# Kernel optimization log

Hardware: AMD Instinct MI355X
Metric: run time of the kernel (lower is better)

## Reference

```python
import jax, jax.numpy as jnp
import numpy as np

N = 20000      # total nodes
E = 320000     # edges (before self loops)
B = 8          # graphs in batch
F_IN = 100
HID = 256
HEADS = 4
DIMS = [(256, 256), (256, 128), (128, 64), (64, 32)]  # (in_dim, out_dim) per level
NEG_SLOPE = 0.2
LN_EPS = 1e-5


def _glorot(k, shape):
    fan = shape[0] + shape[-1]
    return jax.random.normal(k, shape, jnp.float32) * jnp.sqrt(2.0 / fan)


def setup_inputs() -> dict:
    key = jax.random.key(0)
    ks = jax.random.split(key, 32)
    inp = {}
    inp["x"] = jax.random.normal(ks[0], (N, F_IN), jnp.float32)
    inp["edge_index"] = jax.random.randint(ks[1], (2, E), 0, N)
    inp["batch"] = jnp.sort(jax.random.randint(ks[2], (N,), 0, B))
    inp["W_in"] = _glorot(ks[3], (F_IN, HID))
    inp["b_in"] = jnp.zeros((HID,), jnp.float32)
    i = 4
    for l, (di, do) in enumerate(DIMS):
        inp[f"W{l}"] = _glorot(ks[i], (di, HEADS * do)); i += 1
        inp[f"as{l}"] = _glorot(ks[i], (HEADS, do)); i += 1
        inp[f"ad{l}"] = _glorot(ks[i], (HEADS, do)); i += 1
        inp[f"b{l}"] = jnp.zeros((do,), jnp.float32)
        inp[f"g{l}"] = jnp.ones((do,), jnp.float32)
        inp[f"be{l}"] = jnp.zeros((do,), jnp.float32)
    inp["W_out"] = _glorot(ks[i], (DIMS[-1][1], 1))
    inp["b_out"] = jnp.zeros((1,), jnp.float32)
    return inp


def _gat(x, src, dst, W, a_s, a_d, b):
    # PyG GATConv, heads=HEADS, concat=False (head mean), bias after mean
    h = (x @ W).reshape(N, HEADS, -1)              # [N,H,C]
    al_s = (h * a_s).sum(-1)                        # [N,H]
    al_d = (h * a_d).sum(-1)                        # [N,H]
    e = jax.nn.leaky_relu(al_s[src] + al_d[dst], NEG_SLOPE)  # [Etot,H]
    m = jax.ops.segment_max(e, dst, num_segments=N)
    m = jnp.where(jnp.isfinite(m), m, 0.0)
    ex = jnp.exp(e - m[dst])
    den = jax.ops.segment_sum(ex, dst, num_segments=N)
    alpha = ex / (den[dst] + 1e-16)                 # segment softmax over incoming edges
    out = jax.ops.segment_sum(alpha[:, :, None] * h[src], dst, num_segments=N)
    return out.mean(axis=1) + b                     # [N,C]


def _ln(x, g, b):
    mu = x.mean(-1, keepdims=True)
    var = ((x - mu) ** 2).mean(-1, keepdims=True)
    return (x - mu) * jax.lax.rsqrt(var + LN_EPS) * g + b


def _forward(x, edge_index, batch, W_in, b_in, level_params, W_out, b_out):
    loop = jnp.arange(N)
    src = jnp.concatenate([edge_index[0], loop])    # add self loops (GATConv default)
    dst = jnp.concatenate([edge_index[1], loop])
    h = jax.nn.relu(x @ W_in + b_in)
    for (di, do), (W, a_s, a_d, b, g, be) in zip(DIMS, level_params):
        out = _gat(h, src, dst, W, a_s, a_d, b)
        out = jax.nn.relu(out)
        out = _ln(out, g, be)
        # dropout is identity in eval mode
        if di == do:
            out = out + h
        h = out
    cnt = jax.ops.segment_sum(jnp.ones((N,), h.dtype), batch, num_segments=B)
    pooled = jax.ops.segment_sum(h, batch, num_segments=B) / jnp.maximum(cnt, 1.0)[:, None]
    return (pooled @ W_out + b_out)[:, 0]           # [B]


def reference(x, edge_index, batch, W_in, b_in,
              W0, as0, ad0, b0, g0, be0,
              W1, as1, ad1, b1, g1, be1,
              W2, as2, ad2, b2, g2, be2,
              W3, as3, ad3, b3, g3, be3,
              W_out, b_out):
    level_params = [
        (W0, as0, ad0, b0, g0, be0),
        (W1, as1, ad1, b1, g1, be1),
        (W2, as2, ad2, b2, g2, be2),
        (W3, as3, ad3, b3, g3, be3),
    ]
    return _forward(x, edge_index, batch, W_in, b_in, level_params, W_out, b_out)
```

## Files before the change

kernel.cpp:

```cpp
#include <hip/hip_runtime.h>
#include <hip/hip_bf16.h>
#include <cstdint>

constexpr int NN   = 20000;
constexpr int NNP  = 20032;
constexpr int NE   = 320000;
constexpr int ETOT = NE + NN;
constexpr int BG   = 8;
constexpr int FIN  = 100;
constexpr int HID  = 256;
constexpr int H    = 4;
constexpr float SLOPE  = 0.2f;
constexpr float LN_EPS = 1e-5f;

#define DEVFN __device__ __forceinline__

typedef __bf16 bf16x8 __attribute__((ext_vector_type(8)));
typedef float  f32x4  __attribute__((ext_vector_type(4)));
typedef float  f32x2  __attribute__((ext_vector_type(2)));

DEVFN float lrelu(float v) { return v > 0.f ? v : SLOPE * v; }
DEVFN ushort f2bf(float f) {
    unsigned u = __float_as_uint(f);
    return (ushort)((u + 0x7fffu + ((u >> 16) & 1u)) >> 16);
}
DEVFN float bf_lo(unsigned u) { return __uint_as_float(u << 16); }
DEVFN float bf_hi(unsigned u) { return __uint_as_float(u & 0xffff0000u); }
DEVFN float bf2f(unsigned u) { return __uint_as_float(u << 16); }

__global__ void zero_u32(uint32_t* __restrict__ p, int n) {
    int i = blockIdx.x * blockDim.x + threadIdx.x;
    if (i < n) p[i] = 0u;
}

__global__ void scan_kernel(const int* __restrict__ deg, int* __restrict__ rowptr) {
    __shared__ int wsum[16];
    __shared__ int woff[16];
    __shared__ int ctot;
    const int lane = threadIdx.x & 63;
    const int wv   = threadIdx.x >> 6;
    int carry = 0;
    for (int base = 0; base < NN; base += 1024) {
        int i = base + threadIdx.x;
        int v = (i < NN) ? deg[i] : 0;
        int s = v;
#pragma unroll
        for (int off = 1; off < 64; off <<= 1) {
            int t = __shfl_up(s, off);
            if (lane >= off) s += t;
        }
        if (lane == 63) wsum[wv] = s;
        __syncthreads();
        if (wv == 0 && lane < 16) {
            int ws = wsum[lane];
            int sc = ws;
#pragma unroll
            for (int off = 1; off < 16; off <<= 1) {
                int t = __shfl_up(sc, off);
                if (lane >= off) sc += t;
            }
            woff[lane] = sc - ws;
            if (lane == 15) ctot = sc;
        }
        __syncthreads();
        if (i < NN) rowptr[i] = carry + woff[wv] + (s - v);
        carry += ctot;
        __syncthreads();
    }
    if (threadIdx.x == 0) rowptr[NN] = carry;
}

__global__ void scatter_edges(const int* __restrict__ ei, const int* __restrict__ rowptr,
                              int* __restrict__ fill, int* __restrict__ esrc) {
    int k = blockIdx.x * blockDim.x + threadIdx.x;
    if (k >= ETOT) return;
    int s, d;
    if (k < NE) { s = ei[k]; d = ei[NE + k]; }
    else        { s = k - NE; d = k - NE; }
    int pos = rowptr[d] + atomicAdd(&fill[d], 1);
    esrc[pos] = s;
}

constexpr int CXN  = NN * 128;
constexpr int CWI  = 256 * 128;
constexpr int CW0  = 1024 * 256;
constexpr int CW1  = 512 * 256;
constexpr int CW2  = 256 * 128;
constexpr int CW3  = 128 * 64;
constexpr int CTOT = CXN + CWI + CW0 + CW1 + CW2 + CW3;
constexpr int CALL = CTOT + ETOT;

__global__ void conv_all(const float* __restrict__ x, const float* __restrict__ Wi,
                         const float* __restrict__ W0, const float* __restrict__ W1,
                         const float* __restrict__ W2, const float* __restrict__ W3,
                         const int* __restrict__ ei, int* __restrict__ deg,
                         ushort* __restrict__ xpad, ushort* __restrict__ wti,
                         ushort* __restrict__ wt0, ushort* __restrict__ wt1,
                         ushort* __restrict__ wt2, ushort* __restrict__ wt3) {
    int id = blockIdx.x * blockDim.x + threadIdx.x;
    if (id < CXN) {
        int n = id >> 7, k = id & 127;
        xpad[id] = (k < FIN) ? f2bf(x[(size_t)n * FIN + k]) : (ushort)0;
        return;
    }
    id -= CXN;
    if (id < CWI) { int n = id / 128, k = id - n * 128;
        wti[id] = (k < FIN) ? f2bf(Wi[(size_t)k * 256 + n]) : (ushort)0; return; }
    id -= CWI;
    if (id < CW0) { int n = id / 256, k = id - n * 256;
        wt0[id] = f2bf(W0[(size_t)k * 1024 + n]); return; }
    id -= CW0;
    if (id < CW1) { int n = id / 256, k = id - n * 256;
        wt1[id] = f2bf(W1[(size_t)k * 512 + n]); return; }
    id -= CW1;
    if (id < CW2) { int n = id / 128, k = id - n * 128;
        wt2[id] = f2bf(W2[(size_t)k * 256 + n]); return; }
    id -= CW2;
    if (id < CW3) { int n = id / 64, k = id - n * 64;
        wt3[id] = f2bf(W3[(size_t)k * 128 + n]); return; }
    id -= CW3;
    if (id < ETOT) {
        int d = (id < NE) ? ei[NE + id] : (id - NE);
        atomicAdd(&deg[d], 1);
    }
}

template <int K, int NC, int CT, bool BR, bool AL>
__launch_bounds__(256)
__global__ void gemm_mfma(const ushort* __restrict__ A, const ushort* __restrict__ Wt,
                          const float* __restrict__ bias, void* __restrict__ Cout,
                          const float* __restrict__ a_s, const float* __restrict__ a_d,
                          float* __restrict__ al_s, float* __restrict__ al_d, int M) {
    constexpr int LDK = K + 8;
    constexpr int DO_AL = NC / H;
    __shared__ ushort Bs[64 * LDK];
    const int row0 = blockIdx.x * 64;
    const int colbase = blockIdx.y * (64 * CT);
    const int tid = threadIdx.x;
    constexpr int CH = K / 8;
    const int wave = tid >> 6;
    const int lane = tid & 63;
    const int m = lane & 15;
    const int q = lane >> 4;
    const ushort* Ap  = A + (size_t)(row0 + wave * 16 + m) * K + q * 8;
    const ushort* bp0 = &Bs[(0 * 16 + m) * LDK + q * 8];
    const ushort* bp1 = &Bs[(1 * 16 + m) * LDK + q * 8];
    const ushort* bp2 = &Bs[(2 * 16 + m) * LDK + q * 8];
    const ushort* bp3 = &Bs[(3 * 16 + m) * LDK + q * 8];
    const int grow0 = row0 + wave * 16 + q * 4;

    for (int ct = 0; ct < CT; ct++) {
        const int col0 = colbase + ct * 64;
        for (int c = tid; c < 64 * CH; c += 256) {
            int r = c / CH, cc = c - r * CH;
            *(uint4*)(&Bs[r * LDK + cc * 8]) =
                *(const uint4*)(Wt + (size_t)(col0 + r) * K + cc * 8);
        }
        __syncthreads();
        f32x4 acc0 = {0.f, 0.f, 0.f, 0.f}, acc1 = acc0, acc2 = acc0, acc3 = acc0;
#pragma unroll
        for (int kk = 0; kk < K / 32; kk++) {
            bf16x8 a = *(const bf16x8*)(Ap + kk * 32);
            acc0 = __builtin_amdgcn_mfma_f32_16x16x32_bf16(a, *(const bf16x8*)(bp0 + kk * 32), acc0, 0, 0, 0);
            acc1 = __builtin_amdgcn_mfma_f32_16x16x32_bf16(a, *(const bf16x8*)(bp1 + kk * 32), acc1, 0, 0, 0);
            acc2 = __builtin_amdgcn_mfma_f32_16x16x32_bf16(a, *(const bf16x8*)(bp2 + kk * 32), acc2, 0, 0, 0);
            acc3 = __builtin_amdgcn_mfma_f32_16x16x32_bf16(a, *(const bf16x8*)(bp3 + kk * 32), acc3, 0, 0, 0);
        }
        if (!AL) {
            ushort* Cb = (ushort*)Cout + (size_t)grow0 * NC + col0 + m;
            float b0 = 0, b1 = 0, b2 = 0, b3 = 0;
            if (BR) {
                b0 = bias[col0 + m];      b1 = bias[col0 + m + 16];
                b2 = bias[col0 + m + 32]; b3 = bias[col0 + m + 48];
            }
#pragma unroll
            for (int r = 0; r < 4; r++) {
                if (grow0 + r < M) {
                    float v0 = acc0[r], v1 = acc1[r], v2 = acc2[r], v3 = acc3[r];
                    if (BR) {
                        v0 = fmaxf(v0 + b0, 0.f); v1 = fmaxf(v1 + b1, 0.f);
                        v2 = fmaxf(v2 + b2, 0.f); v3 = fmaxf(v3 + b3, 0.f);
                    }
                    Cb[(size_t)r * NC + 0]  = f2bf(v0);
                    Cb[(size_t)r * NC + 16] = f2bf(v1);
                    Cb[(size_t)r * NC + 32] = f2bf(v2);
                    Cb[(size_t)r * NC + 48] = f2bf(v3);
                }
            }
        } else {
            uchar* Cb = (uchar*)Cout + (size_t)grow0 * NC + col0 + m;
#pragma unroll
            for (int r = 0; r < 4; r++) {
                if (grow0 + r < M) {
                    int pk01 = __builtin_amdgcn_cvt_pk_fp8_f32(acc0[r], acc1[r], 0, false);
                    int pk23 = __builtin_amdgcn_cvt_pk_fp8_f32(acc2[r], acc3[r], 0, false);
                    Cb[(size_t)r * NC + 0]  = (uchar)(pk01 & 0xff);
                    Cb[(size_t)r * NC + 16] = (uchar)((pk01 >> 8) & 0xff);
                    Cb[(size_t)r * NC + 32] = (uchar)(pk23 & 0xff);
                    Cb[(size_t)r * NC + 48] = (uchar)((pk23 >> 8) & 0xff);
                }
            }
            float asv[4], adv[4];
#pragma unroll
            for (int t = 0; t < 4; t++) {
                int gc = col0 + m + 16 * t;
                asv[t] = a_s[gc];
                adv[t] = a_d[gc];
            }
            const int h_lo = col0 / DO_AL;
            const int h_hi = (col0 + 32) / DO_AL;
#pragma unroll
            for (int r = 0; r < 4; r++) {
                float ps0 = acc0[r] * asv[0] + acc1[r] * asv[1];
                float ps1 = acc2[r] * asv[2] + acc3[r] * asv[3];
                float pd0 = acc0[r] * adv[0] + acc1[r] * adv[1];
                float pd1 = acc2[r] * adv[2] + acc3[r] * adv[3];
#pragma unroll
                for (int off = 1; off < 16; off <<= 1) {
                    ps0 += __shfl_xor(ps0, off);
                    ps1 += __shfl_xor(ps1, off);
                    pd0 += __shfl_xor(pd0, off);
                    pd1 += __shfl_xor(pd1, off);
                }
                if (m == 0 && grow0 + r < M) {
                    if (h_lo == h_hi) {
                        atomicAdd(&al_s[(grow0 + r) * H + h_lo], ps0 + ps1);
                        atomicAdd(&al_d[(grow0 + r) * H + h_lo], pd0 + pd1);
                    } else {
                        atomicAdd(&al_s[(grow0 + r) * H + h_lo], ps0);
                        atomicAdd(&al_s[(grow0 + r) * H + h_hi], ps1);
                        atomicAdd(&al_d[(grow0 + r) * H + h_lo], pd0);
                        atomicAdd(&al_d[(grow0 + r) * H + h_hi], pd1);
                    }
                }
            }
        }
        __syncthreads();
    }
}

__global__ void softmax_csr(const int* __restrict__ rowptr, const int* __restrict__ esrc,
                            const float* __restrict__ al_s, const float* __restrict__ al_d,
                            float4* __restrict__ alpha) {
    int wid = (blockIdx.x * blockDim.x + threadIdx.x) >> 6;
    int lane = threadIdx.x & 63;
    if (wid >= NN) return;
    int p0 = rowptr[wid], p1 = rowptr[wid + 1];
    float4 d4 = ((const float4*)al_d)[wid];
    float m0 = -1e30f, m1 = -1e30f, m2 = -1e30f, m3 = -1e30f;
    for (int p = p0 + lane; p < p1; p += 64) {
        int s = esrc[p];
        float4 s4 = ((const float4*)al_s)[s];
        m0 = fmaxf(m0, lrelu(s4.x + d4.x));
        m1 = fmaxf(m1, lrelu(s4.y + d4.y));
        m2 = fmaxf(m2, lrelu(s4.z + d4.z));
        m3 = fmaxf(m3, lrelu(s4.w + d4.w));
    }
#pragma unroll
    for (int off = 32; off > 0; off >>= 1) {
        m0 = fmaxf(m0, __shfl_xor(m0, off));
        m1 = fmaxf(m1, __shfl_xor(m1, off));
        m2 = fmaxf(m2, __shfl_xor(m2, off));
        m3 = fmaxf(m3, __shfl_xor(m3, off));
    }
    float s0 = 0.f, s1 = 0.f, s2 = 0.f, s3 = 0.f;
    for (int p = p0 + lane; p < p1; p += 64) {
        int s = esrc[p];
        float4 s4 = ((const float4*)al_s)[s];
        s0 += __expf(lrelu(s4.x + d4.x) - m0);
        s1 += __expf(lrelu(s4.y + d4.y) - m1);
        s2 += __expf(lrelu(s4.z + d4.z) - m2);
        s3 += __expf(lrelu(s4.w + d4.w) - m3);
    }
#pragma unroll
    for (int off = 32; off > 0; off >>= 1) {
        s0 += __shfl_xor(s0, off);
        s1 += __shfl_xor(s1, off);
        s2 += __shfl_xor(s2, off);
        s3 += __shfl_xor(s3, off);
    }
    float i0 = 0.25f / (s0 + 1e-16f), i1 = 0.25f / (s1 + 1e-16f);
    float i2 = 0.25f / (s2 + 1e-16f), i3 = 0.25f / (s3 + 1e-16f);
    for (int p = p0 + lane; p < p1; p += 64) {
        int s = esrc[p];
        float4 s4 = ((const float4*)al_s)[s];
        alpha[p] = make_float4(__expf(lrelu(s4.x + d4.x) - m0) * i0,
                               __expf(lrelu(s4.y + d4.y) - m1) * i1,
                               __expf(lrelu(s4.z + d4.z) - m2) * i2,
                               __expf(lrelu(s4.w + d4.w) - m3) * i3);
    }
}

template <int DO, bool RESID>
__launch_bounds__(256)
__global__ void aggregate(const uchar* __restrict__ hproj, const int* __restrict__ rowptr,
                          const int* __restrict__ esrc, const float4* __restrict__ alpha,
                          const float* __restrict__ bias, const float* __restrict__ gamma,
                          const float* __restrict__ beta, const ushort* __restrict__ hprev,
                          ushort* __restrict__ hout) {
    constexpr int HDO = H * DO;
    constexpr int SL  = HDO / 16;
    constexpr int EPI = 64 / SL;
    constexpr int HL  = DO / 16;
    const int wave = threadIdx.x >> 6;
    const int lane = threadIdx.x & 63;
    const int n = blockIdx.x * 4 + wave;
    const int e  = lane / SL;
    const int sl = lane - e * SL;
    const int hsel = sl / HL;
    const int p0 = rowptr[n], p1 = rowptr[n + 1];
    const uint4* hp4 = (const uint4*)hproj;

    f32x2 acc2[8];
#pragma unroll
    for (int j = 0; j < 8; j++) acc2[j] = f32x2{0.f, 0.f};

    auto sel = [&](float4 al) {
        return (hsel == 0) ? al.x : (hsel == 1) ? al.y : (hsel == 2) ? al.z : al.w;
    };
    auto consume = [&](uint4 v, float a) {
        f32x2 ap = {a, a};
        acc2[0] += ap * __builtin_amdgcn_cvt_pk_f32_fp8(v.x, false);
        acc2[1] += ap * __builtin_amdgcn_cvt_pk_f32_fp8(v.x, true);
        acc2[2] += ap * __builtin_amdgcn_cvt_pk_f32_fp8(v.y, false);
        acc2[3] += ap * __builtin_amdgcn_cvt_pk_f32_fp8(v.y, true);
        acc2[4] += ap * __builtin_amdgcn_cvt_pk_f32_fp8(v.z, false);
        acc2[5] += ap * __builtin_amdgcn_cvt_pk_f32_fp8(v.z, true);
        acc2[6] += ap * __builtin_amdgcn_cvt_pk_f32_fp8(v.w, false);
        acc2[7] += ap * __builtin_amdgcn_cvt_pk_f32_fp8(v.w, true);
    };

    int p = p0 + e;
    bool va = p < p1;
    bool vb = (p + EPI) < p1;
    float aa = 0.f, ab = 0.f;
    uint4 ua = make_uint4(0, 0, 0, 0), ub = make_uint4(0, 0, 0, 0);
    if (va) { aa = sel(alpha[p]);       ua = hp4[(size_t)esrc[p] * SL + sl]; }
    if (vb) { ab = sel(alpha[p + EPI]); ub = hp4[(size_t)esrc[p + EPI] * SL + sl]; }

    while (__any(va)) {
        int pa = p + 2 * EPI, pb = p + 3 * EPI;
        bool va2 = pa < p1, vb2 = pb < p1;
        float aa2 = 0.f, ab2 = 0.f;
        uint4 ua2 = make_uint4(0, 0, 0, 0), ub2 = make_uint4(0, 0, 0, 0);
        if (va2) { aa2 = sel(alpha[pa]); ua2 = hp4[(size_t)esrc[pa] * SL + sl]; }
        if (vb2) { ab2 = sel(alpha[pb]); ub2 = hp4[(size_t)esrc[pb] * SL + sl]; }
        if (va) consume(ua, aa);
        if (vb) consume(ub, ab);
        p = pa; va = va2; vb = vb2; aa = aa2; ab = ab2; ua = ua2; ub = ub2;
    }

    float acc[16];
#pragma unroll
    for (int j = 0; j < 8; j++) { acc[2 * j] = acc2[j][0]; acc[2 * j + 1] = acc2[j][1]; }

#pragma unroll
    for (int off = 32; off >= HL; off >>= 1) {
#pragma unroll
        for (int j = 0; j < 16; j++) acc[j] += __shfl_xor(acc[j], off);
    }
    const int c2 = lane & (HL - 1);
    const int cb = c2 * 16;
    float val[16];
    float s = 0.f;
    {
        float4 b0 = *(const float4*)(bias + cb);
        float4 b1 = *(const float4*)(bias + cb + 4);
        float4 b2 = *(const float4*)(bias + cb + 8);
        float4 b3 = *(const float4*)(bias + cb + 12);
        float bb[16] = {b0.x, b0.y, b0.z, b0.w, b1.x, b1.y, b1.z, b1.w,
                        b2.x, b2.y, b2.z, b2.w, b3.x, b3.y, b3.z, b3.w};
#pragma unroll
        for (int j = 0; j < 16; j++) {
            val[j] = fmaxf(acc[j] + bb[j], 0.f);
            s += val[j];
        }
    }
#pragma unroll
    for (int off = 1; off < HL; off <<= 1) s += __shfl_xor(s, off);
    float mu = s / DO;
    float q = 0.f;
#pragma unroll
    for (int j = 0; j < 16; j++) {
        val[j] -= mu;
        q += val[j] * val[j];
    }
#pragma unroll
    for (int off = 1; off < HL; off <<= 1) q += __shfl_xor(q, off);
    float rstd = rsqrtf(q / DO + LN_EPS);

    if (lane < HL) {
        float4 g0 = *(const float4*)(gamma + cb);
        float4 g1 = *(const float4*)(gamma + cb + 4);
        float4 g2 = *(const float4*)(gamma + cb + 8);
        float4 g3 = *(const float4*)(gamma + cb + 12);
        float4 e0 = *(const float4*)(beta + cb);
        float4 e1 = *(const float4*)(beta + cb + 4);
        float4 e2 = *(const float4*)(beta + cb + 8);
        float4 e3 = *(const float4*)(beta + cb + 12);
        float gg[16] = {g0.x, g0.y, g0.z, g0.w, g1.x, g1.y, g1.z, g1.w,
                        g2.x, g2.y, g2.z, g2.w, g3.x, g3.y, g3.z, g3.w};
        float ee[16] = {e0.x, e0.y, e0.z, e0.w, e1.x, e1.y, e1.z, e1.w,
                        e2.x, e2.y, e2.z, e2.w, e3.x, e3.y, e3.z, e3.w};
        float o[16];
#pragma unroll
        for (int j = 0; j < 16; j++) o[j] = val[j] * rstd * gg[j] + ee[j];
        if (RESID) {
            const uint4* pv = (const uint4*)(hprev + (size_t)n * DO + cb);
            uint4 r0 = pv[0], r1 = pv[1];
            unsigned rr[8] = {r0.x, r0.y, r0.z, r0.w, r1.x, r1.y, r1.z, r1.w};
#pragma unroll
            for (int j = 0; j < 8; j++) {
                o[2 * j]     += bf_lo(rr[j]);
                o[2 * j + 1] += bf_hi(rr[j]);
            }
        }
        unsigned w[8];
#pragma unroll
        for (int j = 0; j < 8; j++)
            w[j] = (unsigned)f2bf(o[2 * j]) | ((unsigned)f2bf(o[2 * j + 1]) << 16);
        uint4* op = (uint4*)(hout + (size_t)n * DO + cb);
        op[0] = make_uint4(w[0], w[1], w[2], w[3]);
        op[1] = make_uint4(w[4], w[5], w[6], w[7]);
    }
}

__global__ void pool_accum2(const ushort* __restrict__ h, const int* __restrict__ batch,
                            float* __restrict__ pooled, float* __restrict__ cnt) {
    __shared__ float lp[BG * 32];
    __shared__ float lc[BG];
    for (int i = threadIdx.x; i < BG * 32; i += blockDim.x) lp[i] = 0.f;
    if (threadIdx.x < BG) lc[threadIdx.x] = 0.f;
    __syncthreads();
    int c = threadIdx.x & 31;
    int rb = threadIdx.x >> 5;
    for (int n = blockIdx.x * 8 + rb; n < NN; n += gridDim.x * 8) {
        int b = batch[n];
        atomicAdd(&lp[b * 32 + c], bf2f((unsigned)h[(size_t)n * 32 + c]));
        if (c == 0) atomicAdd(&lc[b], 1.f);
    }
    __syncthreads();
    for (int i = threadIdx.x; i < BG * 32; i += blockDim.x) atomicAdd(&pooled[i], lp[i]);
    if (threadIdx.x < BG) atomicAdd(&cnt[threadIdx.x], lc[threadIdx.x]);
}

__global__ void final_out(const float* __restrict__ pooled, const float* __restrict__ cnt,
                          const float* __restrict__ Wo, const float* __restrict__ bo,
                          float* __restrict__ out) {
    int b = threadIdx.x;
    if (b < BG) {
        float inv = 1.f / fmaxf(cnt[b], 1.f);
        float acc = 0.f;
        for (int c = 0; c < 32; c++) acc += pooled[b * 32 + c] * inv * Wo[c];
        out[b] = acc + bo[0];
    }
}

extern "C" void kernel_launch(void* const* d_in, const int* in_sizes, int n_in,
                              void* d_out, int out_size, void* d_ws, size_t ws_size,
                              hipStream_t stream) {
    const float* x     = (const float*)d_in[0];
    const int*   ei    = (const int*)d_in[1];
    const int*   batch = (const int*)d_in[2];
    const float* Wi    = (const float*)d_in[3];
    const float* bi    = (const float*)d_in[4];
    const float* Wl[4]  = {(const float*)d_in[5],  (const float*)d_in[11], (const float*)d_in[17], (const float*)d_in[23]};
    const float* Asl[4] = {(const float*)d_in[6],  (const float*)d_in[12], (const float*)d_in[18], (const float*)d_in[24]};
    const float* Adl[4] = {(const float*)d_in[7],  (const float*)d_in[13], (const float*)d_in[19], (const float*)d_in[25]};
    const float* Bl[4]  = {(const float*)d_in[8],  (const float*)d_in[14], (const float*)d_in[20], (const float*)d_in[26]};
    const float* Gl[4]  = {(const float*)d_in[9],  (const float*)d_in[15], (const float*)d_in[21], (const float*)d_in[27]};
    const float* Bel[4] = {(const float*)d_in[10], (const float*)d_in[16], (const float*)d_in[22], (const float*)d_in[28]};
    const float* Wo = (const float*)d_in[29];
    const float* bo = (const float*)d_in[30];

    char* p = (char*)d_ws;
    auto take = [&](size_t bytes) -> void* {
        void* r = (void*)p;
        p += (bytes + 255) & ~(size_t)255;
        return r;
    };
    ushort*   hAbf   = (ushort*)take((size_t)NNP * HID * 2);
    ushort*   hBbf   = (ushort*)take((size_t)NNP * HID * 2);
    uchar*    hproj  = (uchar*)take((size_t)NN * H * HID);
    ushort*   xpad   = (ushort*)take((size_t)NNP * 128 * 2);
    int*      rowptr = (int*)take((size_t)(NN + 1) * 4);
    int*      esrc   = (int*)take((size_t)ETOT * 4);
    float4*   alpha  = (float4*)take((size_t)ETOT * 16);
    ushort*   wti    = (ushort*)take((size_t)CWI * 2);
    ushort*   wt0    = (ushort*)take((size_t)CW0 * 2);
    ushort*   wt1    = (ushort*)take((size_t)CW1 * 2);
    ushort*   wt2    = (ushort*)take((size_t)CW2 * 2);
    ushort*   wt3    = (ushort*)take((size_t)CW3 * 2);
    char*     zbase  = p;
    int*      deg    = (int*)take((size_t)NN * 4);
    int*      fill   = (int*)take((size_t)NN * 4);
    float*    pooled = (float*)take((size_t)BG * 32 * 4);
    float*    cnt    = (float*)take((size_t)BG * 4);
    float*    als[4], *ald[4];
    for (int l = 0; l < 4; l++) {
        als[l] = (float*)take((size_t)NN * H * 4);
        ald[l] = (float*)take((size_t)NN * H * 4);
    }
    const int zcount = (int)((p - zbase) / 4);
    (void)ws_size; (void)n_in; (void)in_sizes; (void)out_size;

    const int ZB = 256;
    const int egrid = (ETOT + ZB - 1) / ZB;
    const int mtiles = (NN + 63) / 64;
    const int sgrid = (NN * 64 + 255) / 256;
    const int agrid = NN / 4;

    zero_u32<<<(zcount + ZB - 1) / ZB, ZB, 0, stream>>>((uint32_t*)zbase, zcount);
    conv_all<<<(CALL + ZB - 1) / ZB, ZB, 0, stream>>>(x, Wi, Wl[0], Wl[1], Wl[2], Wl[3],
                                                      ei, deg,
                                                      xpad, wti, wt0, wt1, wt2, wt3);
    scan_kernel<<<1, 1024, 0, stream>>>(deg, rowptr);
    scatter_edges<<<egrid, ZB, 0, stream>>>(ei, rowptr, fill, esrc);

    gemm_mfma<128, 256, 2, true, false><<<dim3(mtiles, 2), 256, 0, stream>>>(
        xpad, wti, bi, hAbf, nullptr, nullptr, nullptr, nullptr, NN);

    gemm_mfma<256, 1024, 4, false, true><<<dim3(mtiles, 4), 256, 0, stream>>>(
        hAbf, wt0, nullptr, hproj, Asl[0], Adl[0], als[0], ald[0], NN);
    softmax_csr<<<sgrid, 256, 0, stream>>>(rowptr, esrc, als[0], ald[0], alpha);
    aggregate<256, true><<<agrid, 256, 0, stream>>>(hproj, rowptr, esrc, alpha,
                                                    Bl[0], Gl[0], Bel[0], hAbf, hBbf);
    gemm_mfma<256, 512, 4, false, true><<<dim3(mtiles, 2), 256, 0, stream>>>(
        hBbf, wt1, nullptr, hproj, Asl[1], Adl[1], als[1], ald[1], NN);
    softmax_csr<<<sgrid, 256, 0, stream>>>(rowptr, esrc, als[1], ald[1], alpha);
    aggregate<128, false><<<agrid, 256, 0, stream>>>(hproj, rowptr, esrc, alpha,
                                                     Bl[1], Gl[1], Bel[1], nullptr, hAbf);
    gemm_mfma<128, 256, 2, false, true><<<dim3(mtiles, 2), 256, 0, stream>>>(
        hAbf, wt2, nullptr, hproj, Asl[2], Adl[2], als[2], ald[2], NN);
    softmax_csr<<<sgrid, 256, 0, stream>>>(rowptr, esrc, als[2], ald[2], alpha);
    aggregate<64, false><<<agrid, 256, 0, stream>>>(hproj, rowptr, esrc, alpha,
                                                    Bl[2], Gl[2], Bel[2], nullptr, hBbf);
    gemm_mfma<64, 128, 1, false, true><<<dim3(mtiles, 2), 256, 0, stream>>>(
        hBbf, wt3, nullptr, hproj, Asl[3], Adl[3], als[3], ald[3], NN);
    softmax_csr<<<sgrid, 256, 0, stream>>>(rowptr, esrc, als[3], ald[3], alpha);
    aggregate<32, false><<<agrid, 256, 0, stream>>>(hproj, rowptr, esrc, alpha,
                                                    Bl[3], Gl[3], Bel[3], nullptr, hAbf);

    pool_accum2<<<80, 256, 0, stream>>>(hAbf, batch, pooled, cnt);
    final_out<<<1, 64, 0, stream>>>(pooled, cnt, Wo, bo, (float*)d_out);
}
```

Baseline: 537.3 us.

## Prefetch next weight tile into registers in GEMM and vectorize degree scan

The MFMA GEMM now loads the next 64-column weight tile from global memory into registers while the current tile is being computed, then writes it to LDS at the start of the next iteration. The goal is to hide global-load latency behind the MFMA work. It also adds a min-blocks-per-CU hint to the launch bounds. The scan kernel reads degrees as int4 and writes four row pointers per thread, cutting the number of loop passes. The costs are extra register pressure from the prefetch buffer (NB uint4 values, up to 8 for K=256), and the occupancy hint may cause register spills.

```diff
diff --git a/kernel.cpp b/kernel.cpp
--- a/kernel.cpp
+++ b/kernel.cpp
@@ -39,11 +39,14 @@
     __shared__ int ctot;
     const int lane = threadIdx.x & 63;
     const int wv   = threadIdx.x >> 6;
+    const int4* deg4 = (const int4*)deg;
     int carry = 0;
-    for (int base = 0; base < NN; base += 1024) {
-        int i = base + threadIdx.x;
-        int v = (i < NN) ? deg[i] : 0;
-        int s = v;
+    for (int base4 = 0; base4 < NN / 4; base4 += 1024) {
+        int i4 = base4 + threadIdx.x;
+        int4 v = make_int4(0, 0, 0, 0);
+        if (i4 < NN / 4) v = deg4[i4];
+        int t0 = v.x, t1 = t0 + v.y, t2 = t1 + v.z, t3 = t2 + v.w;
+        int s = t3;
 #pragma unroll
         for (int off = 1; off < 64; off <<= 1) {
             int t = __shfl_up(s, off);
@@ -63,7 +66,13 @@
             if (lane == 15) ctot = sc;
         }
         __syncthreads();
-        if (i < NN) rowptr[i] = carry + woff[wv] + (s - v);
+        if (i4 < NN / 4) {
+            int be = carry + woff[wv] + (s - t3);
+            rowptr[4 * i4 + 0] = be;
+            rowptr[4 * i4 + 1] = be + t0;
+            rowptr[4 * i4 + 2] = be + t1;
+            rowptr[4 * i4 + 3] = be + t2;
+        }
         carry += ctot;
         __syncthreads();
     }
@@ -126,18 +135,19 @@
 }
 
 template <int K, int NC, int CT, bool BR, bool AL>
-__launch_bounds__(256)
+__launch_bounds__(256, 4)
 __global__ void gemm_mfma(const ushort* __restrict__ A, const ushort* __restrict__ Wt,
                           const float* __restrict__ bias, void* __restrict__ Cout,
                           const float* __restrict__ a_s, const float* __restrict__ a_d,
                           float* __restrict__ al_s, float* __restrict__ al_d, int M) {
     constexpr int LDK = K + 8;
     constexpr int DO_AL = NC / H;
+    constexpr int CH = K / 8;
+    constexpr int NB = (64 * CH) / 256;
     __shared__ ushort Bs[64 * LDK];
     const int row0 = blockIdx.x * 64;
     const int colbase = blockIdx.y * (64 * CT);
     const int tid = threadIdx.x;
-    constexpr int CH = K / 8;
     const int wave = tid >> 6;
     const int lane = tid & 63;
     const int m = lane & 15;
@@ -149,14 +159,31 @@
     const ushort* bp3 = &Bs[(3 * 16 + m) * LDK + q * 8];
     const int grow0 = row0 + wave * 16 + q * 4;
 
+    uint4 breg[NB];
+#pragma unroll
+    for (int j = 0; j < NB; j++) {
+        int i = j * 256 + tid;
+        int r = i / CH, cc = i - r * CH;
+        breg[j] = *(const uint4*)(Wt + (size_t)(colbase + r) * K + cc * 8);
+    }
+
     for (int ct = 0; ct < CT; ct++) {
         const int col0 = colbase + ct * 64;
-        for (int c = tid; c < 64 * CH; c += 256) {
-            int r = c / CH, cc = c - r * CH;
-            *(uint4*)(&Bs[r * LDK + cc * 8]) =
-                *(const uint4*)(Wt + (size_t)(col0 + r) * K + cc * 8);
+#pragma unroll
+        for (int j = 0; j < NB; j++) {
+            int i = j * 256 + tid;
+            int r = i / CH, cc = i - r * CH;
+            *(uint4*)(&Bs[r * LDK + cc * 8]) = breg[j];
         }
         __syncthreads();
+        if (ct + 1 < CT) {
+#pragma unroll
+            for (int j = 0; j < NB; j++) {
+                int i = j * 256 + tid;
+                int r = i / CH, cc = i - r * CH;
+                breg[j] = *(const uint4*)(Wt + (size_t)(col0 + 64 + r) * K + cc * 8);
+            }
+        }
         f32x4 acc0 = {0.f, 0.f, 0.f, 0.f}, acc1 = acc0, acc2 = acc0, acc3 = acc0;
 #pragma unroll
         for (int kk = 0; kk < K / 32; kk++) {
```

New measurement: 584.5 us. 8.8% more time.
